# Performance work log

Measured on AMD Instinct MI355X. Metric: run time of the kernel, lower is better.

The kernel has to match this reference:

```python
import jax, jax.numpy as jnp
import numpy as np

EMBED_DIM = 1024
EPS = 1e-6


def setup_inputs() -> dict:
    key = jax.random.key(0)
    ks = jax.random.split(key, 9)
    L, B, E = 2048, 4, EMBED_DIM
    s = 1.0 / np.sqrt(E)
    return {
        "query": jax.random.normal(ks[0], (L, B, E), jnp.float32),
        "key": jax.random.normal(ks[1], (L, B, E), jnp.float32),
        "value": jax.random.normal(ks[2], (L, B, E), jnp.float32),
        "Wq": jax.random.normal(ks[3], (E, E), jnp.float32) * s,
        "bq": jnp.zeros((E,), jnp.float32),
        "Wk": jax.random.normal(ks[4], (E, E), jnp.float32) * s,
        "bk": jnp.zeros((E,), jnp.float32),
        "Wv": jax.random.normal(ks[5], (E, E), jnp.float32) * s,
        "bv": jnp.zeros((E,), jnp.float32),
    }


def reference(query, key, value, Wq, bq, Wk, bk, Wv, bv):
    # query: (L, B, E); key/value: (S, B, E)
    L, B, E = query.shape
    S = key.shape[0]
    m = max(L, S)  # static

    # projections + relu feature map, then (B, T, E) layout
    q = jax.nn.relu(jnp.einsum("lbe,fe->lbf", query, Wq) + bq).transpose(1, 0, 2)
    k = jax.nn.relu(jnp.einsum("sbe,fe->sbf", key, Wk) + bk).transpose(1, 0, 2)
    v = (jnp.einsum("sbe,fe->sbf", value, Wv) + bv).transpose(1, 0, 2)

    # cosFormer positional weights: (pi/2) * (i+1) / m, i in [0, T)
    half_pi = jnp.float32(np.pi / 2)
    q_idx = (half_pi * jnp.arange(1, L + 1, dtype=jnp.float32) / m)[None, :, None]
    k_idx = (half_pi * jnp.arange(1, S + 1, dtype=jnp.float32) / m)[None, :, None]

    q_ = jnp.concatenate([q * jnp.sin(q_idx), q * jnp.cos(q_idx)], axis=-1)  # (B, L, 2E)
    k_ = jnp.concatenate([k * jnp.sin(k_idx), k * jnp.cos(k_idx)], axis=-1)  # (B, S, 2E)

    # linear attention: kv_ state (B, E, 2E), normalizer z_ (B, L)
    kv_ = jnp.einsum("nsd,nsm->nmd", k_, v)
    z_ = 1.0 / jnp.maximum(jnp.einsum("nld,nd->nl", q_, k_.sum(axis=1)), EPS)
    attn = jnp.einsum("nld,nmd,nl->nlm", q_, kv_, z_)  # (B, L, E)
    return attn.transpose(1, 0, 2)  # (L, B, E)
```

## Files before the change

kernel.cpp:

```cpp
#include <hip/hip_runtime.h>
#include <hip/hip_fp16.h>


typedef _Float16 f16;
typedef f16 f16x8 __attribute__((ext_vector_type(8)));
typedef f16 f16x4 __attribute__((ext_vector_type(4)));
typedef float f32x4 __attribute__((ext_vector_type(4)));

#define AS1 __attribute__((address_space(1)))
#define AS3 __attribute__((address_space(3)))

__device__ __forceinline__ void gload_lds16(const void* g, void* l) {
  __builtin_amdgcn_global_load_lds((const AS1 void*)g, (AS3 void*)l, 16, 0, 0);
}

__device__ __forceinline__ void xcd_swz(int& bx, int& by, int& bz) {
  const int nx = gridDim.x, ny = gridDim.y;
  const int p = blockIdx.x + nx * (blockIdx.y + ny * blockIdx.z);
  const int chunk = (nx * ny * gridDim.z) >> 3;
  const int l = (p & 7) * chunk + (p >> 3);
  bx = l % nx;
  by = (l / nx) % ny;
  bz = l / (nx * ny);
}

__global__ void cvt3(const float* __restrict__ s0, const float* __restrict__ s1,
                     const float* __restrict__ s2, f16* __restrict__ d0,
                     f16* __restrict__ d1, f16* __restrict__ d2, int n4) {
  const int z = blockIdx.z;
  const float* s = (z == 0) ? s0 : (z == 1) ? s1 : s2;
  f16* d = (z == 0) ? d0 : (z == 1) ? d1 : d2;
  const int i = blockIdx.x * 256 + threadIdx.x;
  if (i >= n4) return;
  const float4 v = ((const float4*)s)[i];
  f16x4 o = { (f16)v.x, (f16)v.y, (f16)v.z, (f16)v.w };
  ((f16x4*)d)[i] = o;
}

__device__ __forceinline__ void mm_core(const f16* __restrict__ A, int lda,
                                        const f16* __restrict__ B, int ldb,
                                        int K, int m0, int n0,
                                        f16* As, f16* Bs, f32x4 (&acc)[4][4]) {
  const int tid  = threadIdx.x;
  const int lane = tid & 63;
  const int w    = tid >> 6;
  const int wm   = w >> 1, wn = w & 1;
  const int l15  = lane & 15;
  const int quad = lane >> 4;

  const f16* ag[4];
  const f16* bg[4];
  f16* al[4];
  f16* bl[4];
#pragma unroll
  for (int i = 0; i < 4; ++i) {
    const int bid = w * 4 + i;
    const int mt = bid >> 1;
    const int kt = bid & 1;
    ag[i] = A + (long)(m0 + mt * 16 + l15) * lda + kt * 32 + quad * 8;
    bg[i] = B + (long)(n0 + mt * 16 + l15) * ldb + kt * 32 + quad * 8;
    al[i] = As + bid * 512;
    bl[i] = Bs + bid * 512;
  }

  for (int k0 = 0; k0 < K; k0 += 64) {
#pragma unroll
    for (int i = 0; i < 4; ++i) {
      gload_lds16(ag[i], al[i]);
      gload_lds16(bg[i], bl[i]);
    }
#pragma unroll
    for (int i = 0; i < 4; ++i) { ag[i] += 64; bg[i] += 64; }
    __syncthreads();
#pragma unroll
    for (int kt = 0; kt < 2; ++kt) {
      f16x8 af[4], bf[4];
#pragma unroll
      for (int i = 0; i < 4; ++i)
        af[i] = *(const f16x8*)(As + ((wm * 4 + i) * 2 + kt) * 512 + lane * 8);
#pragma unroll
      for (int j = 0; j < 4; ++j)
        bf[j] = *(const f16x8*)(Bs + ((wn * 4 + j) * 2 + kt) * 512 + lane * 8);
#pragma unroll
      for (int i = 0; i < 4; ++i)
#pragma unroll
        for (int j = 0; j < 4; ++j)
          acc[i][j] = __builtin_amdgcn_mfma_f32_16x16x32_f16(af[i], bf[j], acc[i][j], 0, 0, 0);
    }
    __syncthreads();
  }
}

__launch_bounds__(256)
__global__ void proj_gemm(const f16* __restrict__ q16, const f16* __restrict__ k16,
                          const f16* __restrict__ v16, const f16* __restrict__ wq,
                          const f16* __restrict__ wk, const f16* __restrict__ wv,
                          const float* __restrict__ bq, const float* __restrict__ bk,
                          const float* __restrict__ bv,
                          f16* __restrict__ Qf, f16* __restrict__ Kn, f16* __restrict__ Vp) {
  __shared__ f16 As[16 * 512];
  __shared__ f16 Bs[16 * 512];
  int bx, by, z;
  xcd_swz(bx, by, z);
  const f16* A = (z == 0) ? q16 : (z == 1) ? k16 : v16;
  const f16* B = (z == 0) ? wq : (z == 1) ? wk : wv;
  const float* bias = (z == 0) ? bq : (z == 1) ? bk : bv;
  const int m0 = by * 128;
  const int n0 = bx * 128;

  f32x4 acc[4][4] = {};
  mm_core(A, 1024, B, 1024, 1024, m0, n0, As, Bs, acc);

  const int tid  = threadIdx.x;
  const int lane = tid & 63;
  const int w    = tid >> 6;
  const int wm   = w >> 1, wn = w & 1;
  const int l15  = lane & 15;
  const int quad = lane >> 4;

  if (z < 2) {
    f16* C = (z == 0) ? Qf : Kn;
    const int ldc = 2048, halfw = 1024;
#pragma unroll
    for (int i = 0; i < 4; ++i) {
      const int mg = m0 + wm * 64 + i * 16 + quad * 4;
      float sn[4], cn[4];
#pragma unroll
      for (int rr = 0; rr < 4; ++rr) {
        const int l = (mg + rr) >> 2;
        const float ang = 7.6699039394282066e-4f * (float)(l + 1);
        __sincosf(ang, &sn[rr], &cn[rr]);
      }
#pragma unroll
      for (int j = 0; j < 4; ++j) {
        const int ng = n0 + wn * 64 + j * 16 + l15;
        const float bc = bias[ng];
#pragma unroll
        for (int rr = 0; rr < 4; ++rr) {
          const float v = fmaxf(acc[i][j][rr] + bc, 0.f);
          C[(long)(mg + rr) * ldc + ng]         = (f16)(v * sn[rr]);
          C[(long)(mg + rr) * ldc + ng + halfw] = (f16)(v * cn[rr]);
        }
      }
    }
  } else {
    f16* C = Vp;
    const int ldc = 1024;
#pragma unroll
    for (int i = 0; i < 4; ++i) {
      const int mg = m0 + wm * 64 + i * 16 + quad * 4;
#pragma unroll
      for (int j = 0; j < 4; ++j) {
        const int ng = n0 + wn * 64 + j * 16 + l15;
        const float bc = bias[ng];
#pragma unroll
        for (int rr = 0; rr < 4; ++rr)
          C[(long)(mg + rr) * ldc + ng] = (f16)(acc[i][j][rr] + bc);
      }
    }
  }
}

template<int MODE>
__launch_bounds__(256)
__global__ void gemm_bt(const f16* __restrict__ A, int lda,
                        const f16* __restrict__ B, int ldb,
                        void* __restrict__ Cout, int K, int ldc,
                        const float* __restrict__ zvec,
                        long abatch, long bbatch, long cbatch)
{
  __shared__ f16 As[16 * 512];
  __shared__ f16 Bs[16 * 512];
  int bx, by, bz;
  xcd_swz(bx, by, bz);
  A += (long)bz * abatch;
  B += (long)bz * bbatch;
  const int m0 = by * 128;
  const int n0 = bx * 128;

  f32x4 acc[4][4] = {};
  mm_core(A, lda, B, ldb, K, m0, n0, As, Bs, acc);

  const int tid  = threadIdx.x;
  const int lane = tid & 63;
  const int w    = tid >> 6;
  const int wm   = w >> 1, wn = w & 1;
  const int l15  = lane & 15;
  const int quad = lane >> 4;

  if constexpr (MODE == 2) {
    f16* C = (f16*)Cout + (long)bz * cbatch;
#pragma unroll
    for (int i = 0; i < 4; ++i) {
      const int mg = m0 + wm * 64 + i * 16 + quad * 4;
#pragma unroll
      for (int j = 0; j < 4; ++j) {
        const int ng = n0 + wn * 64 + j * 16 + l15;
#pragma unroll
        for (int rr = 0; rr < 4; ++rr)
          C[(long)(mg + rr) * ldc + ng] = (f16)acc[i][j][rr];
      }
    }
  } else {
    float* C = (float*)Cout + (long)bz * cbatch;
#pragma unroll
    for (int i = 0; i < 4; ++i) {
      const int mg = m0 + wm * 64 + i * 16 + quad * 4;
      float zr[4];
#pragma unroll
      for (int rr = 0; rr < 4; ++rr) zr[rr] = zvec[(long)(mg + rr) * 4 + bz];
#pragma unroll
      for (int j = 0; j < 4; ++j) {
        const int ng = n0 + wn * 64 + j * 16 + l15;
#pragma unroll
        for (int rr = 0; rr < 4; ++rr)
          C[(long)(mg + rr) * ldc + ng] = acc[i][j][rr] * zr[rr];
      }
    }
  }
}

__global__ void transpose_fused(const f16* __restrict__ Kn, f16* __restrict__ Kt,
                                const f16* __restrict__ Vp, f16* __restrict__ Vt) {
  __shared__ f16 tile[64 * 72];
  const int z = blockIdx.z;
  const f16* in;
  f16* out;
  long in_batch, out_batch;
  int ldin, ldout, b;
  if (z < 4) {
    in = Kn; out = Kt; in_batch = 2048; out_batch = 2048L * 2048;
    ldin = 8192; ldout = 2048; b = z;
  } else {
    if (blockIdx.x >= 16) return;
    in = Vp; out = Vt; in_batch = 1024; out_batch = 1024L * 2048;
    ldin = 4096; ldout = 2048; b = z - 4;
  }
  in  += (long)b * in_batch;
  out += (long)b * out_batch;
  const int r0 = blockIdx.y * 64;
  const int c0 = blockIdx.x * 64;
  const int t  = threadIdx.x;
  {
    const int r = t >> 2, cs = (t & 3) * 16;
    const f16* src = in + (long)(r0 + r) * ldin + c0 + cs;
    f16x8 v0 = *(const f16x8*)(src);
    f16x8 v1 = *(const f16x8*)(src + 8);
    *(f16x8*)(tile + r * 72 + cs)     = v0;
    *(f16x8*)(tile + r * 72 + cs + 8) = v1;
  }
  __syncthreads();
  {
    const int c = t >> 2, rs = (t & 3) * 16;
    alignas(16) f16 tmp[16];
#pragma unroll
    for (int j = 0; j < 16; ++j) tmp[j] = tile[(rs + j) * 72 + c];
    f16* dst = out + (long)(c0 + c) * ldout + r0 + rs;
    *(f16x8*)(dst)     = *(const f16x8*)(tmp);
    *(f16x8*)(dst + 8) = *(const f16x8*)(tmp + 8);
  }
}

__global__ void ksum_kernel(const f16* __restrict__ Kt, float* __restrict__ ks) {
  const long row = blockIdx.x;
  const int t = threadIdx.x;
  f16x8 v = *(const f16x8*)(Kt + row * 2048 + t * 8);
  float s = 0.f;
#pragma unroll
  for (int j = 0; j < 8; ++j) s += (float)v[j];
#pragma unroll
  for (int off = 32; off > 0; off >>= 1) s += __shfl_down(s, off, 64);
  __shared__ float red[4];
  if ((t & 63) == 0) red[t >> 6] = s;
  __syncthreads();
  if (t == 0) ks[row] = red[0] + red[1] + red[2] + red[3];
}

__global__ void z_kernel(const f16* __restrict__ Qf, const float* __restrict__ ks,
                         float* __restrict__ zb) {
  const long r = blockIdx.x;
  const int t = threadIdx.x;
  const int b = (int)(r & 3);
  f16x8 q = *(const f16x8*)(Qf + r * 2048 + t * 8);
  const float* kp = ks + b * 2048 + t * 8;
  float s = 0.f;
#pragma unroll
  for (int j = 0; j < 8; ++j) s += (float)q[j] * kp[j];
#pragma unroll
  for (int off = 32; off > 0; off >>= 1) s += __shfl_down(s, off, 64);
  __shared__ float red[4];
  if ((t & 63) == 0) red[t >> 6] = s;
  __syncthreads();
  if (t == 0) zb[r] = 1.f / fmaxf(red[0] + red[1] + red[2] + red[3], 1e-6f);
}

extern "C" void kernel_launch(void* const* d_in, const int* in_sizes, int n_in,
                              void* d_out, int out_size, void* d_ws, size_t ws_size,
                              hipStream_t stream) {
  const float* query = (const float*)d_in[0];
  const float* key_  = (const float*)d_in[1];
  const float* value = (const float*)d_in[2];
  const float* Wq    = (const float*)d_in[3];
  const float* bq    = (const float*)d_in[4];
  const float* Wk    = (const float*)d_in[5];
  const float* bk    = (const float*)d_in[6];
  const float* Wv    = (const float*)d_in[7];
  const float* bv    = (const float*)d_in[8];

  char* ws = (char*)d_ws;
  const size_t MB = 1ull << 20;
  f16* wq16 = (f16*)(ws + 0 * MB);
  f16* wk16 = (f16*)(ws + 2 * MB);
  f16* wv16 = (f16*)(ws + 4 * MB);
  f16* q16  = (f16*)(ws + 6 * MB);
  f16* k16  = (f16*)(ws + 22 * MB);
  f16* v16  = (f16*)(ws + 38 * MB);
  f16* Qf   = (f16*)(ws + 54 * MB);
  f16* Kn   = (f16*)(ws + 86 * MB);
  f16* Vp   = (f16*)(ws + 118 * MB);
  f16* Kt   = (f16*)(ws + 6 * MB);
  f16* Vt   = (f16*)(ws + 38 * MB);
  f16* kvb  = (f16*)(ws + 86 * MB);
  float* ks = (float*)(ws + 102 * MB);
  float* zb = (float*)(ws + 103 * MB);

  cvt3<<<dim3(8192, 1, 3), 256, 0, stream>>>(query, key_, value, q16, k16, v16, 2097152);
  cvt3<<<dim3(1024, 1, 3), 256, 0, stream>>>(Wq, Wk, Wv, wq16, wk16, wv16, 262144);

  proj_gemm<<<dim3(8, 64, 3), 256, 0, stream>>>(q16, k16, v16, wq16, wk16, wv16,
                                                bq, bk, bv, Qf, Kn, Vp);

  transpose_fused<<<dim3(32, 32, 8), 256, 0, stream>>>(Kn, Kt, Vp, Vt);

  ksum_kernel<<<8192, 256, 0, stream>>>(Kt, ks);
  z_kernel<<<8192, 256, 0, stream>>>(Qf, ks, zb);

  gemm_bt<2><<<dim3(16, 8, 4), 256, 0, stream>>>(Vt, 2048, Kt, 2048, kvb, 2048, 2048,
                                                 nullptr, 1024L * 2048, 2048L * 2048, 1024L * 2048);
  gemm_bt<3><<<dim3(8, 16, 4), 256, 0, stream>>>(Qf, 8192, kvb, 2048, d_out, 2048, 4096,
                                                 zb, 2048, 1024L * 2048, 1024);
}
```

Measured before the change: 415.7 us.

## Double-buffer LDS tiles in GEMM core to overlap loads with MFMA

The shared GEMM core now uses two LDS buffers for A and B. While the MFMAs consume one buffer, the next K-tile is loaded into the other with direct global-to-LDS loads, and there is one barrier per tile instead of two. This aims to hide global load latency behind compute. It doubles LDS use per block from 32KB to 64KB, which can cut occupancy, and the loop assumes the K tile count behaves correctly when odd.

```diff
diff --git a/kernel.cpp b/kernel.cpp
--- a/kernel.cpp
+++ b/kernel.cpp
@@ -40,7 +40,8 @@
 __device__ __forceinline__ void mm_core(const f16* __restrict__ A, int lda,
                                         const f16* __restrict__ B, int ldb,
                                         int K, int m0, int n0,
-                                        f16* As, f16* Bs, f32x4 (&acc)[4][4]) {
+                                        f16* As0, f16* Bs0, f16* As1, f16* Bs1,
+                                        f32x4 (&acc)[4][4]) {
   const int tid  = threadIdx.x;
   const int lane = tid & 63;
   const int w    = tid >> 6;
@@ -50,8 +51,7 @@
 
   const f16* ag[4];
   const f16* bg[4];
-  f16* al[4];
-  f16* bl[4];
+  int lofs[4];
 #pragma unroll
   for (int i = 0; i < 4; ++i) {
     const int bid = w * 4 + i;
@@ -59,34 +59,47 @@
     const int kt = bid & 1;
     ag[i] = A + (long)(m0 + mt * 16 + l15) * lda + kt * 32 + quad * 8;
     bg[i] = B + (long)(n0 + mt * 16 + l15) * ldb + kt * 32 + quad * 8;
-    al[i] = As + bid * 512;
-    bl[i] = Bs + bid * 512;
-  }
-
-  for (int k0 = 0; k0 < K; k0 += 64) {
-#pragma unroll
-    for (int i = 0; i < 4; ++i) {
-      gload_lds16(ag[i], al[i]);
-      gload_lds16(bg[i], bl[i]);
+    lofs[i] = bid * 512;
+  }
+
+  auto STAGE = [&](f16* Asb, f16* Bsb) {
+#pragma unroll
+    for (int i = 0; i < 4; ++i) {
+      gload_lds16(ag[i], Asb + lofs[i]);
+      gload_lds16(bg[i], Bsb + lofs[i]);
     }
 #pragma unroll
     for (int i = 0; i < 4; ++i) { ag[i] += 64; bg[i] += 64; }
-    __syncthreads();
+  };
+
+  auto COMPUTE = [&](const f16* Ab, const f16* Bb) {
 #pragma unroll
     for (int kt = 0; kt < 2; ++kt) {
       f16x8 af[4], bf[4];
 #pragma unroll
       for (int i = 0; i < 4; ++i)
-        af[i] = *(const f16x8*)(As + ((wm * 4 + i) * 2 + kt) * 512 + lane * 8);
+        af[i] = *(const f16x8*)(Ab + ((wm * 4 + i) * 2 + kt) * 512 + lane * 8);
 #pragma unroll
       for (int j = 0; j < 4; ++j)
-        bf[j] = *(const f16x8*)(Bs + ((wn * 4 + j) * 2 + kt) * 512 + lane * 8);
+        bf[j] = *(const f16x8*)(Bb + ((wn * 4 + j) * 2 + kt) * 512 + lane * 8);
 #pragma unroll
       for (int i = 0; i < 4; ++i)
 #pragma unroll
         for (int j = 0; j < 4; ++j)
           acc[i][j] = __builtin_amdgcn_mfma_f32_16x16x32_f16(af[i], bf[j], acc[i][j], 0, 0, 0);
     }
+  };
+
+  STAGE(As0, Bs0);
+  __syncthreads();
+
+  const int nt = K >> 6;
+  for (int t = 0; t < nt; t += 2) {
+    if (t + 1 < nt) STAGE(As1, Bs1);
+    COMPUTE(As0, Bs0);
+    __syncthreads();
+    if (t + 2 < nt) STAGE(As0, Bs0);
+    COMPUTE(As1, Bs1);
     __syncthreads();
   }
 }
@@ -98,8 +111,10 @@
                           const float* __restrict__ bq, const float* __restrict__ bk,
                           const float* __restrict__ bv,
                           f16* __restrict__ Qf, f16* __restrict__ Kn, f16* __restrict__ Vp) {
-  __shared__ f16 As[16 * 512];
-  __shared__ f16 Bs[16 * 512];
+  __shared__ f16 As0[16 * 512];
+  __shared__ f16 Bs0[16 * 512];
+  __shared__ f16 As1[16 * 512];
+  __shared__ f16 Bs1[16 * 512];
   int bx, by, z;
   xcd_swz(bx, by, z);
   const f16* A = (z == 0) ? q16 : (z == 1) ? k16 : v16;
@@ -109,7 +124,7 @@
   const int n0 = bx * 128;
 
   f32x4 acc[4][4] = {};
-  mm_core(A, 1024, B, 1024, 1024, m0, n0, As, Bs, acc);
+  mm_core(A, 1024, B, 1024, 1024, m0, n0, As0, Bs0, As1, Bs1, acc);
 
   const int tid  = threadIdx.x;
   const int lane = tid & 63;
@@ -169,8 +184,10 @@
                         const float* __restrict__ zvec,
                         long abatch, long bbatch, long cbatch)
 {
-  __shared__ f16 As[16 * 512];
-  __shared__ f16 Bs[16 * 512];
+  __shared__ f16 As0[16 * 512];
+  __shared__ f16 Bs0[16 * 512];
+  __shared__ f16 As1[16 * 512];
+  __shared__ f16 Bs1[16 * 512];
   int bx, by, bz;
   xcd_swz(bx, by, bz);
   A += (long)bz * abatch;
@@ -179,7 +196,7 @@
   const int n0 = bx * 128;
 
   f32x4 acc[4][4] = {};
-  mm_core(A, lda, B, ldb, K, m0, n0, As, Bs, acc);
+  mm_core(A, lda, B, ldb, K, m0, n0, As0, Bs0, As1, Bs1, acc);
 
   const int tid  = threadIdx.x;
   const int lane = tid & 63;
```

After: 420.4 us. About the same (+1.1%).

## Pipeline GEMM core with 4-stage LDS ring and 256x128 tiles

Applied to the files above, without the earlier changes.

Rewrites the shared GEMM mainloop into a four-buffer LDS ring that prefetches two K-slices ahead, using partial vmcnt waits and a single barrier per step. Previously each step loaded, synced, computed and synced again. Blocks grow to 512 threads covering 256x128 output tiles, and all GEMM launch grids are halved in M to match. The aim is to hide global-load latency behind MFMA work, at the cost of more LDS per block (96KB) and fewer blocks in flight.

```diff
diff --git a/kernel.cpp b/kernel.cpp
--- a/kernel.cpp
+++ b/kernel.cpp
@@ -40,7 +40,9 @@
 __device__ __forceinline__ void mm_core(const f16* __restrict__ A, int lda,
                                         const f16* __restrict__ B, int ldb,
                                         int K, int m0, int n0,
-                                        f16* As, f16* Bs, f32x4 (&acc)[4][4]) {
+                                        f16* As0, f16* Bs0, f16* As1, f16* Bs1,
+                                        f16* As2, f16* Bs2, f16* As3, f16* Bs3,
+                                        f32x4 (&acc)[4][4]) {
   const int tid  = threadIdx.x;
   const int lane = tid & 63;
   const int w    = tid >> 6;
@@ -48,68 +50,88 @@
   const int l15  = lane & 15;
   const int quad = lane >> 4;
 
-  const f16* ag[4];
-  const f16* bg[4];
-  f16* al[4];
-  f16* bl[4];
-#pragma unroll
-  for (int i = 0; i < 4; ++i) {
-    const int bid = w * 4 + i;
-    const int mt = bid >> 1;
-    const int kt = bid & 1;
-    ag[i] = A + (long)(m0 + mt * 16 + l15) * lda + kt * 32 + quad * 8;
-    bg[i] = B + (long)(n0 + mt * 16 + l15) * ldb + kt * 32 + quad * 8;
-    al[i] = As + bid * 512;
-    bl[i] = Bs + bid * 512;
-  }
-
-  for (int k0 = 0; k0 < K; k0 += 64) {
-#pragma unroll
-    for (int i = 0; i < 4; ++i) {
-      gload_lds16(ag[i], al[i]);
-      gload_lds16(bg[i], bl[i]);
-    }
-#pragma unroll
-    for (int i = 0; i < 4; ++i) { ag[i] += 64; bg[i] += 64; }
-    __syncthreads();
-#pragma unroll
-    for (int kt = 0; kt < 2; ++kt) {
-      f16x8 af[4], bf[4];
-#pragma unroll
-      for (int i = 0; i < 4; ++i)
-        af[i] = *(const f16x8*)(As + ((wm * 4 + i) * 2 + kt) * 512 + lane * 8);
-#pragma unroll
-      for (int j = 0; j < 4; ++j)
-        bf[j] = *(const f16x8*)(Bs + ((wn * 4 + j) * 2 + kt) * 512 + lane * 8);
-#pragma unroll
-      for (int i = 0; i < 4; ++i)
-#pragma unroll
-        for (int j = 0; j < 4; ++j)
-          acc[i][j] = __builtin_amdgcn_mfma_f32_16x16x32_f16(af[i], bf[j], acc[i][j], 0, 0, 0);
-    }
-    __syncthreads();
-  }
-}
-
-__launch_bounds__(256)
+  const f16* pa0 = A + (long)(m0 + w * 16 + l15) * lda + quad * 8;
+  const f16* pa1 = A + (long)(m0 + (8 + w) * 16 + l15) * lda + quad * 8;
+  const f16* pb0 = B + (long)(n0 + w * 16 + l15) * ldb + quad * 8;
+  int koff = 0;
+
+#define STAGE_(Ab, Bb) do {                        \
+    gload_lds16(pa0 + koff, (Ab) + w * 512);       \
+    gload_lds16(pa1 + koff, (Ab) + (8 + w) * 512); \
+    gload_lds16(pb0 + koff, (Bb) + w * 512);       \
+    koff += 32; } while (0)
+
+#define COMPUTE_(Ab, Bb) do {                                                    \
+    f16x8 af[4], bf[4];                                                          \
+    _Pragma("unroll")                                                            \
+    for (int i = 0; i < 4; ++i)                                                  \
+      af[i] = *(const f16x8*)((Ab) + (wm * 4 + i) * 512 + lane * 8);             \
+    _Pragma("unroll")                                                            \
+    for (int j = 0; j < 4; ++j)                                                  \
+      bf[j] = *(const f16x8*)((Bb) + (wn * 4 + j) * 512 + lane * 8);             \
+    _Pragma("unroll")                                                            \
+    for (int i = 0; i < 4; ++i)                                                  \
+      _Pragma("unroll")                                                          \
+      for (int j = 0; j < 4; ++j)                                                \
+        acc[i][j] = __builtin_amdgcn_mfma_f32_16x16x32_f16(af[i], bf[j],         \
+                                                           acc[i][j], 0, 0, 0); \
+  } while (0)
+
+#define WV3_ asm volatile("s_waitcnt vmcnt(3)" ::: "memory")
+#define WV0_ asm volatile("s_waitcnt vmcnt(0)" ::: "memory")
+#define BARR_ do { __builtin_amdgcn_s_barrier(); __builtin_amdgcn_sched_barrier(0); } while (0)
+
+  STAGE_(As0, Bs0);
+  STAGE_(As1, Bs1);
+
+  const int nt = K >> 5;
+  for (int t = 0; t + 5 < nt; t += 4) {
+    WV3_; BARR_; STAGE_(As2, Bs2); COMPUTE_(As0, Bs0);
+    WV3_; BARR_; STAGE_(As3, Bs3); COMPUTE_(As1, Bs1);
+    WV3_; BARR_; STAGE_(As0, Bs0); COMPUTE_(As2, Bs2);
+    WV3_; BARR_; STAGE_(As1, Bs1); COMPUTE_(As3, Bs3);
+  }
+  WV3_; BARR_; STAGE_(As2, Bs2); COMPUTE_(As0, Bs0);
+  WV3_; BARR_; STAGE_(As3, Bs3); COMPUTE_(As1, Bs1);
+  WV3_; BARR_; COMPUTE_(As2, Bs2);
+  WV0_; BARR_; COMPUTE_(As3, Bs3);
+
+#undef STAGE_
+#undef COMPUTE_
+#undef WV3_
+#undef WV0_
+#undef BARR_
+}
+
+#define GEMM_LDS                                   \
+  __shared__ alignas(16) f16 As0[8192];            \
+  __shared__ alignas(16) f16 Bs0[4096];            \
+  __shared__ alignas(16) f16 As1[8192];            \
+  __shared__ alignas(16) f16 Bs1[4096];            \
+  __shared__ alignas(16) f16 As2[8192];            \
+  __shared__ alignas(16) f16 Bs2[4096];            \
+  __shared__ alignas(16) f16 As3[8192];            \
+  __shared__ alignas(16) f16 Bs3[4096];
+
+__launch_bounds__(512, 2)
 __global__ void proj_gemm(const f16* __restrict__ q16, const f16* __restrict__ k16,
                           const f16* __restrict__ v16, const f16* __restrict__ wq,
                           const f16* __restrict__ wk, const f16* __restrict__ wv,
                           const float* __restrict__ bq, const float* __restrict__ bk,
                           const float* __restrict__ bv,
                           f16* __restrict__ Qf, f16* __restrict__ Kn, f16* __restrict__ Vp) {
-  __shared__ f16 As[16 * 512];
-  __shared__ f16 Bs[16 * 512];
+  GEMM_LDS
   int bx, by, z;
   xcd_swz(bx, by, z);
   const f16* A = (z == 0) ? q16 : (z == 1) ? k16 : v16;
   const f16* B = (z == 0) ? wq : (z == 1) ? wk : wv;
   const float* bias = (z == 0) ? bq : (z == 1) ? bk : bv;
-  const int m0 = by * 128;
+  const int m0 = by * 256;
   const int n0 = bx * 128;
 
   f32x4 acc[4][4] = {};
-  mm_core(A, 1024, B, 1024, 1024, m0, n0, As, Bs, acc);
+  mm_core(A, 1024, B, 1024, 1024, m0, n0,
+          As0, Bs0, As1, Bs1, As2, Bs2, As3, Bs3, acc);
 
   const int tid  = threadIdx.x;
   const int lane = tid & 63;
@@ -162,24 +184,24 @@
 }
 
 template<int MODE>
-__launch_bounds__(256)
+__launch_bounds__(512, 2)
 __global__ void gemm_bt(const f16* __restrict__ A, int lda,
                         const f16* __restrict__ B, int ldb,
                         void* __restrict__ Cout, int K, int ldc,
                         const float* __restrict__ zvec,
                         long abatch, long bbatch, long cbatch)
 {
-  __shared__ f16 As[16 * 512];
-  __shared__ f16 Bs[16 * 512];
+  GEMM_LDS
   int bx, by, bz;
   xcd_swz(bx, by, bz);
   A += (long)bz * abatch;
   B += (long)bz * bbatch;
-  const int m0 = by * 128;
+  const int m0 = by * 256;
   const int n0 = bx * 128;
 
   f32x4 acc[4][4] = {};
-  mm_core(A, lda, B, ldb, K, m0, n0, As, Bs, acc);
+  mm_core(A, lda, B, ldb, K, m0, n0,
+          As0, Bs0, As1, Bs1, As2, Bs2, As3, Bs3, acc);
 
   const int tid  = threadIdx.x;
   const int lane = tid & 63;
@@ -327,7 +349,7 @@
   cvt3<<<dim3(8192, 1, 3), 256, 0, stream>>>(query, key_, value, q16, k16, v16, 2097152);
   cvt3<<<dim3(1024, 1, 3), 256, 0, stream>>>(Wq, Wk, Wv, wq16, wk16, wv16, 262144);
 
-  proj_gemm<<<dim3(8, 64, 3), 256, 0, stream>>>(q16, k16, v16, wq16, wk16, wv16,
+  proj_gemm<<<dim3(8, 32, 3), 512, 0, stream>>>(q16, k16, v16, wq16, wk16, wv16,
                                                 bq, bk, bv, Qf, Kn, Vp);
 
   transpose_fused<<<dim3(32, 32, 8), 256, 0, stream>>>(Kn, Kt, Vp, Vt);
@@ -335,8 +357,8 @@
   ksum_kernel<<<8192, 256, 0, stream>>>(Kt, ks);
   z_kernel<<<8192, 256, 0, stream>>>(Qf, ks, zb);
 
-  gemm_bt<2><<<dim3(16, 8, 4), 256, 0, stream>>>(Vt, 2048, Kt, 2048, kvb, 2048, 2048,
+  gemm_bt<2><<<dim3(16, 4, 4), 512, 0, stream>>>(Vt, 2048, Kt, 2048, kvb, 2048, 2048,
                                                  nullptr, 1024L * 2048, 2048L * 2048, 1024L * 2048);
-  gemm_bt<3><<<dim3(8, 16, 4), 256, 0, stream>>>(Qf, 8192, kvb, 2048, d_out, 2048, 4096,
-                                                 zb, 2048, 1024L * 2048, 1024);
-}
+  gemm_bt<3><<<dim3(8, 8, 4), 512, 0, stream>>>(Qf, 8192, kvb, 2048, d_out, 2048, 4096,
+                                                zb, 2048, 1024L * 2048, 1024);
+}
```

After: 372.7 us. 1.12x faster.
